# Optimization experiments

Measured on AMD Instinct MI355X. Metric: run time of the kernel, lower is better.

## Reference

```python
import jax, jax.numpy as jnp
import numpy as np

NEG_SLOPE_GAT = 0.2   # GATConv internal leaky_relu slope (PyG default)
NEG_SLOPE = 0.01      # nn.LeakyReLU default slope


def _gat(h_src_in, h_dst_in, src, dst, Wsrc, Wdst, a_s, a_d, b, n_dst, self_loops):
    """Single-head PyG-style GATConv: gather -> score -> edge softmax -> scatter-sum."""
    hs = h_src_in @ Wsrc            # [N_src, C]
    hd = h_dst_in @ Wdst            # [N_dst, C]
    if self_loops:                  # static flag; same node set on both sides
        loop = jnp.arange(n_dst, dtype=src.dtype)
        src = jnp.concatenate([src, loop])
        dst = jnp.concatenate([dst, loop])
    # attention logits per edge
    e = jax.nn.leaky_relu((hs @ a_s)[src] + (hd @ a_d)[dst], NEG_SLOPE_GAT)  # [E]
    # softmax over edges sharing a destination node
    m = jax.ops.segment_max(e, dst, num_segments=n_dst)
    ex = jnp.exp(e - m[dst])
    denom = jax.ops.segment_sum(ex, dst, num_segments=n_dst)
    alpha = ex / denom[dst]
    out = jax.ops.segment_sum(hs[src] * alpha[:, None], dst, num_segments=n_dst)
    return out + b


def setup_inputs() -> dict:
    key = jax.random.key(0)
    ks = iter(jax.random.split(key, 64))
    NB, NP = 100_000, 50_000
    E_bb, E_pp, E_bp = 800_000, 400_000, 400_000
    FB, FP, H, H2 = 32, 34, 64, 32
    rn = lambda shape, s=0.05: jax.random.normal(next(ks), shape, jnp.float32) * s
    d = {}
    d['x_b'] = rn((NB, FB), 1.0)
    d['x_p'] = rn((NP, FP), 1.0)
    d['ei_bb'] = jax.random.randint(next(ks), (2, E_bb), 0, NB, jnp.int32)
    d['ei_pp'] = jax.random.randint(next(ks), (2, E_pp), 0, NP, jnp.int32)
    d['ei_bp_src'] = jax.random.randint(next(ks), (E_bp,), 0, NB, jnp.int32)
    d['ei_bp_dst'] = jax.random.randint(next(ks), (E_bp,), 0, NP, jnp.int32)
    d['W_in_b'] = rn((FB, H)); d['b_in_b'] = jnp.zeros((H,), jnp.float32)
    d['W_in_p'] = rn((FP, H)); d['b_in_p'] = jnp.zeros((H,), jnp.float32)
    for tag, cin, cout in (('1', H, H), ('2', H, H2)):
        d['W_bb' + tag] = rn((cin, cout)); d['as_bb' + tag] = rn((cout,)); d['ad_bb' + tag] = rn((cout,)); d['b_bb' + tag] = jnp.zeros((cout,), jnp.float32)
        d['W_pp' + tag] = rn((cin, cout)); d['as_pp' + tag] = rn((cout,)); d['ad_pp' + tag] = rn((cout,)); d['b_pp' + tag] = jnp.zeros((cout,), jnp.float32)
        d['Ws_bp' + tag] = rn((cin, cout)); d['Wd_bp' + tag] = rn((cin, cout)); d['as_bp' + tag] = rn((cout,)); d['ad_bp' + tag] = rn((cout,)); d['b_bp' + tag] = jnp.zeros((cout,), jnp.float32)
    d['W_out'] = rn((H2, 1)); d['b_out'] = jnp.zeros((1,), jnp.float32)
    return d


def reference(x_b, x_p, ei_bb, ei_pp, ei_bp_src, ei_bp_dst,
              W_in_b, b_in_b, W_in_p, b_in_p,
              W_bb1, as_bb1, ad_bb1, b_bb1, W_pp1, as_pp1, ad_pp1, b_pp1,
              Ws_bp1, Wd_bp1, as_bp1, ad_bp1, b_bp1,
              W_bb2, as_bb2, ad_bb2, b_bb2, W_pp2, as_pp2, ad_pp2, b_pp2,
              Ws_bp2, Wd_bp2, as_bp2, ad_bp2, b_bp2,
              W_out, b_out):
    NB, NP = x_b.shape[0], x_p.shape[0]
    lr = lambda v: jax.nn.leaky_relu(v, NEG_SLOPE)
    # input projections (dropout is eval-mode identity)
    hb = lr(x_b @ W_in_b + b_in_b)
    hp = lr(x_p @ W_in_p + b_in_p)
    # hetero conv 1 (sum aggregation over relations sharing a dst type)
    ob = _gat(hb, hb, ei_bb[0], ei_bb[1], W_bb1, W_bb1, as_bb1, ad_bb1, b_bb1, NB, True)
    op = (_gat(hp, hp, ei_pp[0], ei_pp[1], W_pp1, W_pp1, as_pp1, ad_pp1, b_pp1, NP, True)
          + _gat(hb, hp, ei_bp_src, ei_bp_dst, Ws_bp1, Wd_bp1, as_bp1, ad_bp1, b_bp1, NP, False))
    hb, hp = lr(ob), lr(op)
    # hetero conv 2
    ob2 = _gat(hb, hb, ei_bb[0], ei_bb[1], W_bb2, W_bb2, as_bb2, ad_bb2, b_bb2, NB, True)
    op2 = (_gat(hp, hp, ei_pp[0], ei_pp[1], W_pp2, W_pp2, as_pp2, ad_pp2, b_pp2, NP, True)
           + _gat(hb, hp, ei_bp_src, ei_bp_dst, Ws_bp2, Wd_bp2, as_bp2, ad_bp2, b_bp2, NP, False))
    hp = lr(op2)
    return hp @ W_out + b_out  # [NP, 1]
```

## Files before the change

### kernel.cpp

```cpp
#include <hip/hip_runtime.h>
#include <hip/hip_bf16.h>
#include <cstdint>
#include <cstddef>


typedef __attribute__((ext_vector_type(8))) short short8;
typedef __attribute__((ext_vector_type(4))) float f32x4;
typedef unsigned int u32;
typedef __hip_bfloat16 bf16;

#define ABITS 9
#define CHUNKE 4096

static __device__ __forceinline__ float b2f(bf16 v) { return __bfloat162float(v); }

static __device__ __forceinline__ float ldf(const void* p, int i, int bf) {
    return bf ? __bfloat162float(((const bf16*)p)[i]) : ((const float*)p)[i];
}

static __device__ __forceinline__ short f2bs(float f) {
    bf16 h = __float2bfloat16(f);
    return *reinterpret_cast<short*>(&h);
}
static __device__ __forceinline__ float bs2f(short s) {
    bf16 h = *reinterpret_cast<bf16*>(&s);
    return __bfloat162float(h);
}
static __device__ __forceinline__ float lo16(u32 u) { return bs2f((short)(u & 0xffffu)); }
static __device__ __forceinline__ float hi16(u32 u) { return bs2f((short)(u >> 16)); }
static __device__ __forceinline__ u32 pack2(float x, float y) {
    return (u32)(unsigned short)f2bs(x) | ((u32)(unsigned short)f2bs(y) << 16);
}
static __device__ __forceinline__ float sel4(const float* a, int i) {
    return i == 0 ? a[0] : i == 1 ? a[1] : i == 2 ? a[2] : a[3];
}
static __device__ __forceinline__ float lrelu2(float x) { return x > 0.f ? x : 0.2f * x; }

__global__ __launch_bounds__(256) void k_bkt_hist(
    const int* __restrict__ bb_d, const int* __restrict__ pp_d,
    const int* __restrict__ bp_d, int* __restrict__ histM,
    const unsigned* __restrict__ probe_w, int* __restrict__ flag,
    int E_bb, int E_pp, int E_bp, int NB, int NP, int nbkt, int nblk)
{
    if (blockIdx.x == 0) {
        __shared__ int s_cnt;
        if (threadIdx.x == 0) s_cnt = 0;
        __syncthreads();
        int c = 0;
#pragma unroll
        for (int j = 0; j < 4; ++j) {
            unsigned u = probe_w[threadIdx.x * 4 + j];
            unsigned e = (u >> 7) & 0xffu;
            c += (e >= 100u && e <= 145u) ? 1 : 0;
        }
        atomicAdd(&s_cnt, c);
        __syncthreads();
        if (threadIdx.x == 0) *flag = (s_cnt > 614) ? 1 : 0;
    }
    __shared__ int h[1 << ABITS];
    for (int i = threadIdx.x; i < nbkt; i += 256) h[i] = 0;
    __syncthreads();
    int E_all = E_bb + E_pp + E_bp;
    int base = blockIdx.x * CHUNKE;
    int end = base + CHUNKE < E_all ? base + CHUNKE : E_all;
    for (int i = base + threadIdx.x; i < end; i += 256) {
        int d;
        if (i < E_bb) d = bb_d[i];
        else if (i < E_bb + E_pp) d = NB + pp_d[i - E_bb];
        else d = NB + NP + bp_d[i - E_bb - E_pp];
        atomicAdd(&h[d >> ABITS], 1);
    }
    __syncthreads();
    for (int i = threadIdx.x; i < nbkt; i += 256)
        histM[(size_t)i * nblk + blockIdx.x] = h[i];
}

__global__ __launch_bounds__(1024) void k_scan1(const int* __restrict__ deg,
                                                int* __restrict__ out,
                                                int* __restrict__ bsum, int n)
{
    __shared__ int wsum[16];
    int gid = blockIdx.x * 1024 + threadIdx.x;
    int lane = threadIdx.x & 63, wid = threadIdx.x >> 6;
    int v = (gid < n) ? deg[gid] : 0;
    int x = v;
#pragma unroll
    for (int off = 1; off < 64; off <<= 1) {
        int y = __shfl_up(x, off, 64);
        if (lane >= off) x += y;
    }
    if (lane == 63) wsum[wid] = x;
    __syncthreads();
    if (wid == 0 && lane < 16) {
        int w0 = wsum[lane];
#pragma unroll
        for (int off = 1; off < 16; off <<= 1) {
            int y = __shfl_up(w0, off, 16);
            if (lane >= off) w0 += y;
        }
        wsum[lane] = w0;
    }
    __syncthreads();
    int base = (wid > 0) ? wsum[wid - 1] : 0;
    int incl = base + x;
    if (gid < n) out[gid] = incl - v;
    if (threadIdx.x == 1023) bsum[blockIdx.x] = incl;
}

__global__ __launch_bounds__(1024) void k_scan2(int* __restrict__ bsum, int nb)
{
    __shared__ int wsum[16];
    int lane = threadIdx.x & 63, wid = threadIdx.x >> 6;
    int v = (threadIdx.x < nb) ? bsum[threadIdx.x] : 0;
    int x = v;
#pragma unroll
    for (int off = 1; off < 64; off <<= 1) {
        int y = __shfl_up(x, off, 64);
        if (lane >= off) x += y;
    }
    if (lane == 63) wsum[wid] = x;
    __syncthreads();
    if (wid == 0 && lane < 16) {
        int w0 = wsum[lane];
#pragma unroll
        for (int off = 1; off < 16; off <<= 1) {
            int y = __shfl_up(w0, off, 16);
            if (lane >= off) w0 += y;
        }
        wsum[lane] = w0;
    }
    __syncthreads();
    int base = (wid > 0) ? wsum[wid - 1] : 0;
    if (threadIdx.x < nb) bsum[threadIdx.x] = base + x - v;
}

__global__ __launch_bounds__(1024) void k_scan3(int* __restrict__ indptr,
                                                const int* __restrict__ bsum,
                                                int n, int E)
{
    int gid = blockIdx.x * 1024 + threadIdx.x;
    if (gid < n) indptr[gid] += bsum[blockIdx.x];
    if (gid == 0) indptr[n] = E;
}

__global__ __launch_bounds__(256) void k_bkt_scatter(
    const int* __restrict__ bb_s, const int* __restrict__ bb_d,
    const int* __restrict__ pp_s, const int* __restrict__ pp_d,
    const int* __restrict__ bp_s, const int* __restrict__ bp_d,
    const int* __restrict__ histS, unsigned* __restrict__ ebuf,
    int E_bb, int E_pp, int E_bp, int NB, int NP, int nbkt, int nblk)
{
    __shared__ int cur[1 << ABITS];
    for (int i = threadIdx.x; i < nbkt; i += 256)
        cur[i] = histS[(size_t)i * nblk + blockIdx.x];
    __syncthreads();
    int E_all = E_bb + E_pp + E_bp;
    int base = blockIdx.x * CHUNKE;
    int end = base + CHUNKE < E_all ? base + CHUNKE : E_all;
    for (int i = base + threadIdx.x; i < end; i += 256) {
        int s, d;
        if (i < E_bb) { s = bb_s[i]; d = bb_d[i]; }
        else if (i < E_bb + E_pp) { int j = i - E_bb; s = pp_s[j]; d = NB + pp_d[j]; }
        else { int j = i - E_bb - E_pp; s = bp_s[j]; d = NB + NP + bp_d[j]; }
        int p = atomicAdd(&cur[d >> ABITS], 1);
        ebuf[p] = ((unsigned)(d & ((1 << ABITS) - 1)) << 20) | (unsigned)s;
    }
}

__global__ __launch_bounds__(256) void k_finalize(
    const unsigned* __restrict__ ebuf, const int* __restrict__ histS,
    int* __restrict__ ip_all, int* __restrict__ sidx,
    int NALL, int E_all, int nbkt, int nblk)
{
    __shared__ int h[1 << ABITS];
    __shared__ int pre[1 << ABITS];
    __shared__ int wq[4];
    int b = blockIdx.x;
    int d0 = b << ABITS;
    int nloc = NALL - d0 < (1 << ABITS) ? NALL - d0 : (1 << ABITS);
    int t = threadIdx.x;
    for (int i = t; i < (1 << ABITS); i += 256) h[i] = 0;
    __syncthreads();
    int s0 = histS[(size_t)b * nblk];
    int s1 = histS[(size_t)(b + 1) * nblk];
    for (int i = s0 + t; i < s1; i += 256)
        atomicAdd(&h[ebuf[i] >> 20], 1);
    __syncthreads();
    int v0 = h[2 * t], v1 = h[2 * t + 1];
    int ps = v0 + v1;
    int lane = t & 63, wid = t >> 6;
    int x = ps;
#pragma unroll
    for (int off = 1; off < 64; off <<= 1) {
        int y = __shfl_up(x, off, 64);
        if (lane >= off) x += y;
    }
    if (lane == 63) wq[wid] = x;
    __syncthreads();
    if (t == 0) {
        int a = 0;
#pragma unroll
        for (int w = 0; w < 4; ++w) { int tmp = wq[w]; wq[w] = a; a += tmp; }
    }
    __syncthreads();
    int excl = wq[wid] + x - ps;
    pre[2 * t]     = excl;
    pre[2 * t + 1] = excl + v0;
    __syncthreads();
    for (int i = t; i < nloc; i += 256) ip_all[d0 + i] = s0 + pre[i];
    if (d0 + nloc == NALL && t == 0) ip_all[NALL] = E_all;
    for (int i = t; i < (1 << ABITS); i += 256) h[i] = s0 + pre[i];
    __syncthreads();
    for (int i = s0 + t; i < s1; i += 256) {
        unsigned e = ebuf[i];
        int p = atomicAdd(&h[e >> 20], 1);
        sidx[p] = (int)(e & 0xFFFFFu);
    }
}

template <int CIN>
static __device__ __forceinline__ void in_proj_body(
    short* WT, float* bl, int bid,
    const void* __restrict__ X, const void* __restrict__ W, const void* __restrict__ B,
    bf16* __restrict__ Y, int M, int bf)
{
    constexpr int KP = 40;
    for (int i = threadIdx.x; i < 64 * CIN; i += 256) {
        int n = i / CIN, k = i - n * CIN;
        WT[n * KP + k] = f2bs(ldf(W, k * 64 + n, bf));
    }
    if (threadIdx.x < 64) bl[threadIdx.x] = ldf(B, threadIdx.x, bf);
    __syncthreads();

    int lane = threadIdx.x & 63;
    int wv   = threadIdx.x >> 6;
    int m = lane & 15, quad = lane >> 4;
    int row0 = (bid * 4 + wv) * 16;
    if (row0 >= M) return;

    int arow = row0 + m; if (arow >= M) arow = M - 1;
    short8 a;
#pragma unroll
    for (int j = 0; j < 8; ++j)
        a[j] = f2bs(ldf(X, arow * CIN + quad * 8 + j, bf));

    f32x4 acc[4] = {};
#pragma unroll
    for (int tt = 0; tt < 4; ++tt) {
        short8 bfr = *(const short8*)&WT[((lane & 15) + 16 * tt) * KP + quad * 8];
        acc[tt] = __builtin_amdgcn_mfma_f32_16x16x32_bf16(a, bfr, acc[tt], 0, 0, 0);
// ... 4 lines not shown
#pragma unroll
        for (int r = 0; r < 4; ++r) {
            int row = row0 + quad * 4 + r; if (row >= M) row = M - 1;
            x32[r] = ldf(X, row * CIN + 32, bf);
            x33[r] = ldf(X, row * CIN + 33, bf);
        }
#pragma unroll
        for (int tt = 0; tt < 4; ++tt) {
            int col = (lane & 15) + 16 * tt;
            float w32 = bs2f(WT[col * KP + 32]);
            float w33 = bs2f(WT[col * KP + 33]);
#pragma unroll
            for (int r = 0; r < 4; ++r)
                acc[tt][r] += x32[r] * w32 + x33[r] * w33;
        }
    }

#pragma unroll
    for (int tt = 0; tt < 4; ++tt) {
        int col = (lane & 15) + 16 * tt;
        float bb = bl[col];
#pragma unroll
        for (int r = 0; r < 4; ++r) {
            int row = row0 + quad * 4 + r;
            if (row < M) {
                float v = acc[tt][r] + bb;
                v = v > 0.f ? v : 0.01f * v;
                Y[(size_t)row * 64 + col] = __float2bfloat16(v);
            }
        }
    }
}

__global__ __launch_bounds__(256) void k_in_proj_all(
    const void* __restrict__ Xb, const void* __restrict__ Wb, const void* __restrict__ Bb,
    bf16* __restrict__ Yb, int MB,
    const void* __restrict__ Xp, const void* __restrict__ Wp, const void* __restrict__ Bp,
    bf16* __restrict__ Yp, int MP, const int* __restrict__ flag)
{
    const int bf = *flag;
    __shared__ short WT[64 * 40];
    __shared__ float bl[64];
    int nbb = (MB + 63) >> 6;
    if (blockIdx.x < nbb) in_proj_body<32>(WT, bl, blockIdx.x, Xb, Wb, Bb, Yb, MB, bf);
    else                  in_proj_body<34>(WT, bl, blockIdx.x - nbb, Xp, Wp, Bp, Yp, MP, bf);
}

template <int N1, int N2, bool S1F, bool S2F>
static __device__ __forceinline__ void dual_body(
    short* WT, int bid, const bf16* __restrict__ H,
    const void* __restrict__ W1, const void* __restrict__ W2,
    const void* __restrict__ as1, const void* __restrict__ ad1,
    const void* __restrict__ as2, const void* __restrict__ ad2,
    bf16* __restrict__ HS1, bf16* __restrict__ HS2,
    float* __restrict__ SS1, float* __restrict__ SD1,
    float* __restrict__ SS2, float* __restrict__ SD2,
    int M, int bf)
{
    constexpr int KP = 72;
    constexpr int T1 = N1 / 16, T2 = N2 / 16, T = T1 + T2;
    for (int i = threadIdx.x; i < N1 * 64; i += 256) {
        int n = i >> 6, k = i & 63;
        WT[n * KP + k] = f2bs(ldf(W1, k * N1 + n, bf));
    }
    for (int i = threadIdx.x; i < N2 * 64; i += 256) {
        int n = i >> 6, k = i & 63;
        WT[(N1 + n) * KP + k] = f2bs(ldf(W2, k * N2 + n, bf));
    }
    __syncthreads();

    int lane = threadIdx.x & 63;
    int wv   = threadIdx.x >> 6;
    int m = lane & 15, quad = lane >> 4;
    int row0 = (bid * 4 + wv) * 16;
    if (row0 >= M) return;

    const short* Hs = (const short*)H;
    int arow = row0 + m; if (arow >= M) arow = M - 1;
// ... 126 lines not shown
            vs[r] += acc[tt][r] * asv[tt];
            vd[r] += acc[tt][r] * adv[tt];
        }
#pragma unroll
    for (int off = 1; off < 16; off <<= 1)
#pragma unroll
        for (int r = 0; r < 4; ++r) {
            vs[r] += __shfl_xor(vs[r], off);
            vd[r] += __shfl_xor(vd[r], off);
        }
    int c = lane & 15;
    if (c < 8) {
        int row = row0 + quad * 4 + (c & 3);
        if (row < M) {
            if (c < 4) SS[row] = sel4(vs, c & 3);
            else       SD[row] = sel4(vd, c & 3);
        }
    }

    if (STORE) {
#pragma unroll
        for (int tt = 0; tt < T; ++tt) {
            int col = (lane & 15) + 16 * tt;
#pragma unroll
            for (int r = 0; r < 4; ++r) {
                int row = row0 + quad * 4 + r;
                if (row < M)
                    HS[(size_t)row * N + col] = __float2bfloat16(acc[tt][r]);
            }
        }
    }
}

__global__ __launch_bounds__(256) void k_dual64_all(
    const bf16* __restrict__ hb,
    const void* W_bb1, const void* Ws_bp1,
    const void* as_bb1, const void* ad_bb1, const void* as_bp1, const void* ad_bp1,
    bf16* hs_bb, bf16* hs_bp,
    float* ss_bb, float* sd_bb, float* ss_bp, float* junkNB, int MB,
    const bf16* __restrict__ hp,
    const void* W_pp1, const void* Wd_bp1,
    const void* as_pp1, const void* ad_pp1,
    bf16* hs_pp, float* ss_pp, float* sd_pp, float* junkNP, float* sd_bp, int MP,
    const int* __restrict__ flag)
{
    const int bf = *flag;
    __shared__ short WT[128 * 72];
    int nbb = (MB + 63) >> 6;
    if (blockIdx.x < nbb)
        dual_body<64, 64, true, true>(WT, blockIdx.x, hb, W_bb1, Ws_bp1,
            as_bb1, ad_bb1, as_bp1, ad_bp1, hs_bb, hs_bp,
            ss_bb, sd_bb, ss_bp, junkNB, MB, bf);
    else
        dual_body<64, 64, true, false>(WT, blockIdx.x - nbb, hp, W_pp1, Wd_bp1,
            as_pp1, ad_pp1, as_bp1, ad_bp1, hs_pp, nullptr,
            ss_pp, sd_pp, junkNP, sd_bp, MP, bf);
}

__global__ __launch_bounds__(256) void k_proj2_all(
    const bf16* __restrict__ hp2,
    const void* W_pp2, const void* Wd_bp2,
    const void* as_pp2, const void* ad_pp2, const void* as_bp2, const void* ad_bp2,
    bf16* hs2_pp, float* ss2_pp, float* sd2_pp, float* junkNP, float* sd2_bp, int MP,
    const bf16* __restrict__ hb2,
    const void* Ws_bp2, bf16* hs2_bp, float* ss2_bp, float* junkNB, int MB,
    const int* __restrict__ flag)
{
    const int bf = *flag;
    __shared__ short WT[64 * 72];
    int npb = (MP + 63) >> 6;
    if (blockIdx.x < npb)
        dual_body<32, 32, true, false>(WT, blockIdx.x, hp2, W_pp2, Wd_bp2,
            as_pp2, ad_pp2, as_bp2, ad_bp2, hs2_pp, nullptr,
            ss2_pp, sd2_pp, junkNP, sd2_bp, MP, bf);
    else
        proj_body<32, true>(WT, blockIdx.x - npb, hb2, Ws_bp2,
            as_bp2, ad_bp2, hs2_bp, ss2_bp, junkNB, MB, bf);
}

static __device__ __forceinline__ void gather1_body(
    int bid, const int* __restrict__ ip, const int* __restrict__ si,
    const float* __restrict__ SS, const float* __restrict__ SD,
    const bf16* __restrict__ HS, const void* __restrict__ bias,
    bf16* __restrict__ OUT, int M, int bf)
{
    int lane = threadIdx.x & 63;
    int half = lane >> 5, hl = lane & 31;
    int d = bid * 4 + (threadIdx.x >> 6);
    if (d >= M) return;
    const u32* H32 = (const u32*)HS;
    float sdd = SD[d];
    float ax = 0.f, ay = 0.f, den = 0.f;
    if (half == 0) {
        float ex = __expf(lrelu2(SS[d] + sdd));
        u32 h = H32[(size_t)d * 32 + hl];
        ax = lo16(h) * ex; ay = hi16(h) * ex; den = ex;
    }
    int j1 = ip[d + 1];
    int j = ip[d] + half;
    for (; j + 2 < j1; j += 4) {
        int s0 = si[j], s1 = si[j + 2];
        u32 h0 = H32[(size_t)s0 * 32 + hl];
        u32 h1 = H32[(size_t)s1 * 32 + hl];
        float e0 = __expf(lrelu2(SS[s0] + sdd));
        float e1 = __expf(lrelu2(SS[s1] + sdd));
        ax += lo16(h0) * e0 + lo16(h1) * e1;
        ay += hi16(h0) * e0 + hi16(h1) * e1;
        den += e0 + e1;
    }
    if (j < j1) {
        int s0 = si[j];
        u32 h0 = H32[(size_t)s0 * 32 + hl];
        float e0 = __expf(lrelu2(SS[s0] + sdd));
        ax += lo16(h0) * e0; ay += hi16(h0) * e0; den += e0;
    }
    ax += __shfl_xor(ax, 32); ay += __shfl_xor(ay, 32); den += __shfl_xor(den, 32);
    if (half == 0) {
        float vx = ax / den + ldf(bias, 2 * hl, bf);
        float vy = ay / den + ldf(bias, 2 * hl + 1, bf);
        vx = vx > 0.f ? vx : 0.01f * vx;
        vy = vy > 0.f ? vy : 0.01f * vy;
        ((u32*)OUT)[(size_t)d * 32 + hl] = pack2(vx, vy);
    }
}

static __device__ __forceinline__ void gather2_body(
    int bid, const int* __restrict__ ip1, const int* __restrict__ si,
    const float* __restrict__ SS1, const float* __restrict__ SD1,
    const bf16* __restrict__ HS1,
    const int* __restrict__ ip2,
    const float* __restrict__ SS2, const float* __restrict__ SD2,
    const bf16* __restrict__ HS2,
    const void* __restrict__ b1, const void* __restrict__ b2,
    bf16* __restrict__ OUT, int M, int bf)
{
    int lane = threadIdx.x & 63;
    int half = lane >> 5, hl = lane & 31;
    int d = bid * 4 + (threadIdx.x >> 6);
    if (d >= M) return;
    const u32* H1 = (const u32*)HS1;
    const u32* H2 = (const u32*)HS2;
    float sdd = SD1[d];
    float a1x = 0.f, a1y = 0.f, den1 = 0.f;
    if (half == 0) {
        float ex = __expf(lrelu2(SS1[d] + sdd));
        u32 h = H1[(size_t)d * 32 + hl];
        a1x = lo16(h) * ex; a1y = hi16(h) * ex; den1 = ex;
    }
    int j1 = ip1[d + 1];
    int j = ip1[d] + half;
    for (; j + 2 < j1; j += 4) {
        int s0 = si[j], s1 = si[j + 2];
        u32 h0 = H1[(size_t)s0 * 32 + hl];
        u32 h1 = H1[(size_t)s1 * 32 + hl];
        float e0 = __expf(lrelu2(SS1[s0] + sdd));
        float e1 = __expf(lrelu2(SS1[s1] + sdd));
        a1x += lo16(h0) * e0 + lo16(h1) * e1;
        a1y += hi16(h0) * e0 + hi16(h1) * e1;
        den1 += e0 + e1;
    }
    if (j < j1) {
        int s0 = si[j];
        u32 h0 = H1[(size_t)s0 * 32 + hl];
        float e0 = __expf(lrelu2(SS1[s0] + sdd));
        a1x += lo16(h0) * e0; a1y += hi16(h0) * e0; den1 += e0;
    }
    float sdd2 = SD2[d];
    float a2x = 0.f, a2y = 0.f, den2 = 0.f;
    j1 = ip2[d + 1];
    j = ip2[d] + half;
    for (; j + 2 < j1; j += 4) {
        int s0 = si[j], s1 = si[j + 2];
        u32 h0 = H2[(size_t)s0 * 32 + hl];
        u32 h1 = H2[(size_t)s1 * 32 + hl];
        float e0 = __expf(lrelu2(SS2[s0] + sdd2));
        float e1 = __expf(lrelu2(SS2[s1] + sdd2));
        a2x += lo16(h0) * e0 + lo16(h1) * e1;
        a2y += hi16(h0) * e0 + hi16(h1) * e1;
        den2 += e0 + e1;
    }
    if (j < j1) {
        int s0 = si[j];
        u32 h0 = H2[(size_t)s0 * 32 + hl];
        float e0 = __expf(lrelu2(SS2[s0] + sdd2));
        a2x += lo16(h0) * e0; a2y += hi16(h0) * e0; den2 += e0;
    }
    a1x += __shfl_xor(a1x, 32); a1y += __shfl_xor(a1y, 32); den1 += __shfl_xor(den1, 32);
    a2x += __shfl_xor(a2x, 32); a2y += __shfl_xor(a2y, 32); den2 += __shfl_xor(den2, 32);
    if (half == 0) {
        float inv2 = den2 > 0.f ? 1.f / den2 : 0.f;
        float vx = a1x / den1 + a2x * inv2 + ldf(b1, 2 * hl, bf) + ldf(b2, 2 * hl, bf);
        float vy = a1y / den1 + a2y * inv2 + ldf(b1, 2 * hl + 1, bf) + ldf(b2, 2 * hl + 1, bf);
        vx = vx > 0.f ? vx : 0.01f * vx;
        vy = vy > 0.f ? vy : 0.01f * vy;
        ((u32*)OUT)[(size_t)d * 32 + hl] = pack2(vx, vy);
    }
}

__global__ __launch_bounds__(256) void k_gather12(
    const int* __restrict__ ip_bb, const int* __restrict__ si,
    const float* __restrict__ ss_bb, const float* __restrict__ sd_bb,
    const bf16* __restrict__ hs_bb, const void* __restrict__ b_bb1,
    bf16* __restrict__ hb2, int NB,
    const int* __restrict__ ip_pp, const int* __restrict__ ip_bp,
    const float* __restrict__ ss_pp, const float* __restrict__ sd_pp,
    const bf16* __restrict__ hs_pp,
    const float* __restrict__ ss_bp, const float* __restrict__ sd_bp,
    const bf16* __restrict__ hs_bp,
    const void* __restrict__ b_pp1, const void* __restrict__ b_bp1,
    bf16* __restrict__ hp2, int NP,
    const int* __restrict__ flag)
{
    const int bf = *flag;
    int nbb = (NB + 3) >> 2;
    if (blockIdx.x < nbb)
        gather1_body(blockIdx.x, ip_bb, si, ss_bb, sd_bb, hs_bb, b_bb1, hb2, NB, bf);
    else
        gather2_body(blockIdx.x - nbb, ip_pp, si, ss_pp, sd_pp, hs_pp,
                     ip_bp, ss_bp, sd_bp, hs_bp, b_pp1, b_bp1, hp2, NP, bf);
}

__global__ __launch_bounds__(256) void k_gather_out(
    const int* __restrict__ ip1, const int* __restrict__ si,
    const float* __restrict__ SS1, const float* __restrict__ SD1,
    const bf16* __restrict__ HS1,
    const int* __restrict__ ip2,
    const float* __restrict__ SS2, const float* __restrict__ SD2,
    const bf16* __restrict__ HS2,
    const void* __restrict__ b1, const void* __restrict__ b2,
    const void* __restrict__ Wout, const void* __restrict__ bout,
    void* __restrict__ OUT, int M, const int* __restrict__ flag)
{
    const int bf = *flag;
    int lane = threadIdx.x & 63;
    int q = lane >> 4, hl = lane & 15;
    int d = blockIdx.x * 4 + (threadIdx.x >> 6);
    if (d >= M) return;
    const u32* H1 = (const u32*)HS1;
    const u32* H2 = (const u32*)HS2;
    float sdd = SD1[d];
    float a1x = 0.f, a1y = 0.f, den1 = 0.f;
    if (q == 0) {
        float ex = __expf(lrelu2(SS1[d] + sdd));
        u32 h = H1[(size_t)d * 16 + hl];
        a1x = lo16(h) * ex; a1y = hi16(h) * ex; den1 = ex;
    }
    int j1 = ip1[d + 1];
    for (int j = ip1[d] + q; j < j1; j += 4) {
        int s0 = si[j];
        u32 h0 = H1[(size_t)s0 * 16 + hl];
        float e0 = __expf(lrelu2(SS1[s0] + sdd));
        a1x += lo16(h0) * e0; a1y += hi16(h0) * e0; den1 += e0;
// ... 41 lines not shown
    const void *W_bb1 = d_in[10], *as_bb1 = d_in[11], *ad_bb1 = d_in[12], *b_bb1 = d_in[13];
    const void *W_pp1 = d_in[14], *as_pp1 = d_in[15], *ad_pp1 = d_in[16], *b_pp1 = d_in[17];
    const void *Ws_bp1 = d_in[18], *Wd_bp1 = d_in[19], *as_bp1 = d_in[20], *ad_bp1 = d_in[21], *b_bp1 = d_in[22];
    const void *W_pp2 = d_in[27], *as_pp2 = d_in[28], *ad_pp2 = d_in[29], *b_pp2 = d_in[30];
    const void *Ws_bp2 = d_in[31], *Wd_bp2 = d_in[32], *as_bp2 = d_in[33], *ad_bp2 = d_in[34], *b_bp2 = d_in[35];
    const void *W_out = d_in[36], *b_out = d_in[37];

    const int NB   = in_sizes[0] / 32;
    const int NP   = in_sizes[1] / 34;
    const int E_bb = in_sizes[2] / 2;
    const int E_pp = in_sizes[3] / 2;
    const int E_bp = in_sizes[4];
    const int E_all = E_bb + E_pp + E_bp;
    const int NALL  = NB + 2 * NP;
    const int* bb_s = ei_bb;  const int* bb_d = ei_bb + E_bb;
    const int* pp_s = ei_pp;  const int* pp_d = ei_pp + E_pp;
    (void)ws_size; (void)n_in; (void)out_size;

    const int nbkt  = (NALL + (1 << ABITS) - 1) >> ABITS;
    const int nblk  = (E_all + CHUNKE - 1) / CHUNKE;
    const int nh    = nbkt * nblk;

    char* base = (char*)d_ws;
    size_t o = 0;
    auto alloc = [&](size_t bytes) { char* p = base + o; o += (bytes + 255) & ~(size_t)255; return p; };

    int* flag  = (int*)alloc(256);
    int* bsum  = (int*)alloc(1024 * 4);
    int* histM = (int*)alloc((size_t)nh * 4);
    int* histS = (int*)alloc((size_t)(nh + 1) * 4);
    int* ip_all = (int*)alloc((size_t)(NALL + 1) * 4);
    unsigned* ebuf = (unsigned*)alloc((size_t)E_all * 4);
    int* si_all = (int*)alloc((size_t)E_all * 4);
    float* ss_bb = (float*)alloc((size_t)NB * 4);
    float* sd_bb = (float*)alloc((size_t)NB * 4);
    float* ss_bp = (float*)alloc((size_t)NB * 4);
    float* ss_pp = (float*)alloc((size_t)NP * 4);
    float* sd_pp = (float*)alloc((size_t)NP * 4);
    float* sd_bp = (float*)alloc((size_t)NP * 4);
    float* ss2_bp = ss_bb;
    float* ss2_pp = ss_pp;
    float* sd2_pp = sd_pp;
    float* sd2_bp = sd_bp;
    float* junkNB = (float*)ebuf;
    float* junkNP = (float*)ebuf + NB;

    char* S1 = alloc((size_t)NB * 64 * 2);
    char* S2 = alloc((size_t)NP * 64 * 2);
    char* S3 = alloc((size_t)NB * 64 * 2);
    char* S4 = alloc((size_t)NB * 64 * 2);
    char* S5 = alloc((size_t)NB * 64 * 2);
    char* S6 = alloc((size_t)NP * 64 * 2);

    bf16* hb     = (bf16*)S1;
    bf16* hp     = (bf16*)S2;
    bf16* hs_bb  = (bf16*)S3;
    bf16* hb2    = (bf16*)S4;
    bf16* hs_bp  = (bf16*)S5;
    bf16* hs_pp  = (bf16*)S6;
    bf16* hp2    = (bf16*)S2;
    bf16* hs2_pp = (bf16*)S3;
    bf16* hs2_bp = (bf16*)S1;

    auto cdiv = [](int a, int b) { return (a + b - 1) / b; };

    k_bkt_hist<<<nblk, 256, 0, stream>>>(bb_d, pp_d, bp_d, histM,
                                         (const unsigned*)x_b, flag,
                                         E_bb, E_pp, E_bp, NB, NP, nbkt, nblk);
    int sb1 = cdiv(nh, 1024);
    k_scan1<<<sb1, 1024, 0, stream>>>(histM, histS, bsum, nh);
    k_scan2<<<1, 1024, 0, stream>>>(bsum, sb1);
    k_scan3<<<sb1, 1024, 0, stream>>>(histS, bsum, nh, E_all);
    k_bkt_scatter<<<nblk, 256, 0, stream>>>(bb_s, bb_d, pp_s, pp_d, bp_s, bp_d,
                                            histS, ebuf, E_bb, E_pp, E_bp, NB, NP, nbkt, nblk);
    k_finalize<<<nbkt, 256, 0, stream>>>(ebuf, histS, ip_all, si_all, NALL, E_all, nbkt, nblk);

    const int* ip_bb = ip_all;
    const int* ip_pp = ip_all + NB;
    const int* ip_bp = ip_all + NB + NP;

    k_in_proj_all<<<cdiv(NB, 64) + cdiv(NP, 64), 256, 0, stream>>>(
        x_b, W_in_b, b_in_b, hb, NB, x_p, W_in_p, b_in_p, hp, NP, flag);

    k_dual64_all<<<cdiv(NB, 64) + cdiv(NP, 64), 256, 0, stream>>>(
        hb, W_bb1, Ws_bp1, as_bb1, ad_bb1, as_bp1, ad_bp1,
        hs_bb, hs_bp, ss_bb, sd_bb, ss_bp, junkNB, NB,
        hp, W_pp1, Wd_bp1, as_pp1, ad_pp1,
        hs_pp, ss_pp, sd_pp, junkNP, sd_bp, NP, flag);

    k_gather12<<<cdiv(NB, 4) + cdiv(NP, 4), 256, 0, stream>>>(
        ip_bb, si_all, ss_bb, sd_bb, hs_bb, b_bb1, hb2, NB,
        ip_pp, ip_bp, ss_pp, sd_pp, hs_pp, ss_bp, sd_bp, hs_bp,
        b_pp1, b_bp1, hp2, NP, flag);

    k_proj2_all<<<cdiv(NP, 64) + cdiv(NB, 64), 256, 0, stream>>>(
        hp2, W_pp2, Wd_bp2, as_pp2, ad_pp2, as_bp2, ad_bp2,
        hs2_pp, ss2_pp, sd2_pp, junkNP, sd2_bp, NP,
        hb2, Ws_bp2, hs2_bp, ss2_bp, junkNB, NB, flag);

    k_gather_out<<<cdiv(NP, 4), 256, 0, stream>>>(
        ip_pp, si_all, ss2_pp, sd2_pp, hs2_pp,
        ip_bp, ss2_bp, sd2_bp, hs2_bp,
        b_pp2, b_bp2, W_out, b_out, d_out, NP, flag);
}
```

Before: 407.9 us.

## Fuse CSR build with projections and precompute layer-1 edge weights in finalize

```diff
diff --git a/kernel.cpp b/kernel.cpp
--- a/kernel.cpp
+++ b/kernel.cpp
@@ -10,7 +10,7 @@
 typedef __hip_bfloat16 bf16;
 
 #define ABITS 9
-#define CHUNKE 4096
+#define CHUNKE 8192
 
 static __device__ __forceinline__ float b2f(bf16 v) { return __bfloat162float(v); }
 
@@ -36,186 +36,21 @@
 }
 static __device__ __forceinline__ float lrelu2(float x) { return x > 0.f ? x : 0.2f * x; }
 
-__global__ __launch_bounds__(256) void k_bkt_hist(
-    const int* __restrict__ bb_d, const int* __restrict__ pp_d,
-    const int* __restrict__ bp_d, int* __restrict__ histM,
-    const unsigned* __restrict__ probe_w, int* __restrict__ flag,
-    int E_bb, int E_pp, int E_bp, int NB, int NP, int nbkt, int nblk)
-{
-    if (blockIdx.x == 0) {
-        __shared__ int s_cnt;
-        if (threadIdx.x == 0) s_cnt = 0;
-        __syncthreads();
-        int c = 0;
-#pragma unroll
-        for (int j = 0; j < 4; ++j) {
-            unsigned u = probe_w[threadIdx.x * 4 + j];
-            unsigned e = (u >> 7) & 0xffu;
-            c += (e >= 100u && e <= 145u) ? 1 : 0;
-        }
-        atomicAdd(&s_cnt, c);
-        __syncthreads();
-        if (threadIdx.x == 0) *flag = (s_cnt > 614) ? 1 : 0;
-    }
-    __shared__ int h[1 << ABITS];
-    for (int i = threadIdx.x; i < nbkt; i += 256) h[i] = 0;
-    __syncthreads();
-    int E_all = E_bb + E_pp + E_bp;
-    int base = blockIdx.x * CHUNKE;
-    int end = base + CHUNKE < E_all ? base + CHUNKE : E_all;
-    for (int i = base + threadIdx.x; i < end; i += 256) {
-        int d;
-        if (i < E_bb) d = bb_d[i];
-        else if (i < E_bb + E_pp) d = NB + pp_d[i - E_bb];
-        else d = NB + NP + bp_d[i - E_bb - E_pp];
-        atomicAdd(&h[d >> ABITS], 1);
-    }
-    __syncthreads();
-    for (int i = threadIdx.x; i < nbkt; i += 256)
-        histM[(size_t)i * nblk + blockIdx.x] = h[i];
-}
-
-__global__ __launch_bounds__(1024) void k_scan1(const int* __restrict__ deg,
-                                                int* __restrict__ out,
-                                                int* __restrict__ bsum, int n)
-{
-    __shared__ int wsum[16];
-    int gid = blockIdx.x * 1024 + threadIdx.x;
-    int lane = threadIdx.x & 63, wid = threadIdx.x >> 6;
-    int v = (gid < n) ? deg[gid] : 0;
-    int x = v;
-#pragma unroll
-    for (int off = 1; off < 64; off <<= 1) {
-        int y = __shfl_up(x, off, 64);
-        if (lane >= off) x += y;
-    }
-    if (lane == 63) wsum[wid] = x;
-    __syncthreads();
-    if (wid == 0 && lane < 16) {
-        int w0 = wsum[lane];
-#pragma unroll
-        for (int off = 1; off < 16; off <<= 1) {
-            int y = __shfl_up(w0, off, 16);
-            if (lane >= off) w0 += y;
-        }
-        wsum[lane] = w0;
-    }
-    __syncthreads();
-    int base = (wid > 0) ? wsum[wid - 1] : 0;
-    int incl = base + x;
-    if (gid < n) out[gid] = incl - v;
-    if (threadIdx.x == 1023) bsum[blockIdx.x] = incl;
-}
-
-__global__ __launch_bounds__(1024) void k_scan2(int* __restrict__ bsum, int nb)
-{
-    __shared__ int wsum[16];
-    int lane = threadIdx.x & 63, wid = threadIdx.x >> 6;
-    int v = (threadIdx.x < nb) ? bsum[threadIdx.x] : 0;
-    int x = v;
-#pragma unroll
-    for (int off = 1; off < 64; off <<= 1) {
-        int y = __shfl_up(x, off, 64);
-        if (lane >= off) x += y;
-    }
-    if (lane == 63) wsum[wid] = x;
-    __syncthreads();
-    if (wid == 0 && lane < 16) {
-        int w0 = wsum[lane];
-#pragma unroll
-        for (int off = 1; off < 16; off <<= 1) {
-            int y = __shfl_up(w0, off, 16);
-            if (lane >= off) w0 += y;
-        }
-        wsum[lane] = w0;
-    }
-    __syncthreads();
-    int base = (wid > 0) ? wsum[wid - 1] : 0;
-    if (threadIdx.x < nb) bsum[threadIdx.x] = base + x - v;
-}
-
-__global__ __launch_bounds__(1024) void k_scan3(int* __restrict__ indptr,
-                                                const int* __restrict__ bsum,
-                                                int n, int E)
-{
-    int gid = blockIdx.x * 1024 + threadIdx.x;
-    if (gid < n) indptr[gid] += bsum[blockIdx.x];
-    if (gid == 0) indptr[n] = E;
-}
-
-__global__ __launch_bounds__(256) void k_bkt_scatter(
-    const int* __restrict__ bb_s, const int* __restrict__ bb_d,
-    const int* __restrict__ pp_s, const int* __restrict__ pp_d,
-    const int* __restrict__ bp_s, const int* __restrict__ bp_d,
-    const int* __restrict__ histS, unsigned* __restrict__ ebuf,
-    int E_bb, int E_pp, int E_bp, int NB, int NP, int nbkt, int nblk)
-{
-    __shared__ int cur[1 << ABITS];
-    for (int i = threadIdx.x; i < nbkt; i += 256)
-        cur[i] = histS[(size_t)i * nblk + blockIdx.x];
-    __syncthreads();
-    int E_all = E_bb + E_pp + E_bp;
-    int base = blockIdx.x * CHUNKE;
-    int end = base + CHUNKE < E_all ? base + CHUNKE : E_all;
-    for (int i = base + threadIdx.x; i < end; i += 256) {
-        int s, d;
-        if (i < E_bb) { s = bb_s[i]; d = bb_d[i]; }
-        else if (i < E_bb + E_pp) { int j = i - E_bb; s = pp_s[j]; d = NB + pp_d[j]; }
-        else { int j = i - E_bb - E_pp; s = bp_s[j]; d = NB + NP + bp_d[j]; }
-        int p = atomicAdd(&cur[d >> ABITS], 1);
-        ebuf[p] = ((unsigned)(d & ((1 << ABITS) - 1)) << 20) | (unsigned)s;
-    }
-}
-
-__global__ __launch_bounds__(256) void k_finalize(
-    const unsigned* __restrict__ ebuf, const int* __restrict__ histS,
-    int* __restrict__ ip_all, int* __restrict__ sidx,
-    int NALL, int E_all, int nbkt, int nblk)
-{
-    __shared__ int h[1 << ABITS];
-    __shared__ int pre[1 << ABITS];
-    __shared__ int wq[4];
-    int b = blockIdx.x;
-    int d0 = b << ABITS;
-    int nloc = NALL - d0 < (1 << ABITS) ? NALL - d0 : (1 << ABITS);
-    int t = threadIdx.x;
-    for (int i = t; i < (1 << ABITS); i += 256) h[i] = 0;
-    __syncthreads();
-    int s0 = histS[(size_t)b * nblk];
-    int s1 = histS[(size_t)(b + 1) * nblk];
-    for (int i = s0 + t; i < s1; i += 256)
-        atomicAdd(&h[ebuf[i] >> 20], 1);
-    __syncthreads();
-    int v0 = h[2 * t], v1 = h[2 * t + 1];
-    int ps = v0 + v1;
-    int lane = t & 63, wid = t >> 6;
-    int x = ps;
-#pragma unroll
-    for (int off = 1; off < 64; off <<= 1) {
-        int y = __shfl_up(x, off, 64);
-        if (lane >= off) x += y;
-    }
-    if (lane == 63) wq[wid] = x;
-    __syncthreads();
-    if (t == 0) {
-        int a = 0;
-#pragma unroll
-        for (int w = 0; w < 4; ++w) { int tmp = wq[w]; wq[w] = a; a += tmp; }
-    }
-    __syncthreads();
-    int excl = wq[wid] + x - ps;
-    pre[2 * t]     = excl;
-    pre[2 * t + 1] = excl + v0;
-    __syncthreads();
-    for (int i = t; i < nloc; i += 256) ip_all[d0 + i] = s0 + pre[i];
-    if (d0 + nloc == NALL && t == 0) ip_all[NALL] = E_all;
-    for (int i = t; i < (1 << ABITS); i += 256) h[i] = s0 + pre[i];
-    __syncthreads();
-    for (int i = s0 + t; i < s1; i += 256) {
-        unsigned e = ebuf[i];
-        int p = atomicAdd(&h[e >> 20], 1);
-        sidx[p] = (int)(e & 0xFFFFFu);
-    }
+static __device__ __forceinline__ int probe_bf(const unsigned* __restrict__ w, int* cnt) {
+    if (threadIdx.x == 0) *cnt = 0;
+    __syncthreads();
+    int c = 0;
+#pragma unroll
+    for (int j = 0; j < 4; ++j) {
+        unsigned u = w[threadIdx.x * 4 + j];
+        unsigned e = (u >> 7) & 0xffu;
+        c += (e >= 100u && e <= 145u) ? 1 : 0;
+    }
+    atomicAdd(cnt, c);
+    __syncthreads();
+    int r = (*cnt > 614) ? 1 : 0;
+    __syncthreads();
+    return r;
 }
 
 template <int CIN>
@@ -286,18 +121,114 @@
     }
 }
 
-__global__ __launch_bounds__(256) void k_in_proj_all(
+__global__ __launch_bounds__(256) void k_hist_inproj(
+    const int* __restrict__ bb_d, const int* __restrict__ pp_d,
+    const int* __restrict__ bp_d, int* __restrict__ histM,
+    const unsigned* __restrict__ probe_w, int* __restrict__ flag,
+    int E_bb, int E_pp, int E_bp, int NB, int NP, int nbkt, int nblk,
     const void* __restrict__ Xb, const void* __restrict__ Wb, const void* __restrict__ Bb,
     bf16* __restrict__ Yb, int MB,
     const void* __restrict__ Xp, const void* __restrict__ Wp, const void* __restrict__ Bp,
-    bf16* __restrict__ Yp, int MP, const int* __restrict__ flag)
-{
-    const int bf = *flag;
+    bf16* __restrict__ Yp, int MP)
+{
     __shared__ short WT[64 * 40];
     __shared__ float bl[64];
-    int nbb = (MB + 63) >> 6;
-    if (blockIdx.x < nbb) in_proj_body<32>(WT, bl, blockIdx.x, Xb, Wb, Bb, Yb, MB, bf);
-    else                  in_proj_body<34>(WT, bl, blockIdx.x - nbb, Xp, Wp, Bp, Yp, MP, bf);
+    __shared__ int aux[1 << ABITS];
+    if ((int)blockIdx.x < nblk) {
+        if (blockIdx.x == 0) {
+            int b = probe_bf(probe_w, &aux[0]);
+            if (threadIdx.x == 0) *flag = b;
+        }
+        for (int i = threadIdx.x; i < nbkt; i += 256) aux[i] = 0;
+        __syncthreads();
+        int E_all = E_bb + E_pp + E_bp;
+        int base = blockIdx.x * CHUNKE;
+        int end = base + CHUNKE < E_all ? base + CHUNKE : E_all;
+        for (int i = base + threadIdx.x; i < end; i += 256) {
+            int d;
+            if (i < E_bb) d = bb_d[i];
+            else if (i < E_bb + E_pp) d = NB + pp_d[i - E_bb];
+            else d = NB + NP + bp_d[i - E_bb - E_pp];
+            atomicAdd(&aux[d >> ABITS], 1);
+        }
+        __syncthreads();
+        for (int i = threadIdx.x; i < nbkt; i += 256)
+            histM[(size_t)i * nblk + blockIdx.x] = aux[i];
+    } else {
+        int bfv = probe_bf(probe_w, &aux[0]);
+        int bid = blockIdx.x - nblk;
+        int nbb = (MB + 63) >> 6;
+        if (bid < nbb) in_proj_body<32>(WT, bl, bid, Xb, Wb, Bb, Yb, MB, bfv);
+        else           in_proj_body<34>(WT, bl, bid - nbb, Xp, Wp, Bp, Yp, MP, bfv);
+    }
+}
+
+__global__ __launch_bounds__(1024) void k_scan1(const int* __restrict__ deg,
+                                                int* __restrict__ out,
+                                                int* __restrict__ bsum, int n)
+{
+    __shared__ int wsum[16];
+    int gid = blockIdx.x * 1024 + threadIdx.x;
+    int lane = threadIdx.x & 63, wid = threadIdx.x >> 6;
+    int v = (gid < n) ? deg[gid] : 0;
+    int x = v;
+#pragma unroll
+    for (int off = 1; off < 64; off <<= 1) {
+        int y = __shfl_up(x, off, 64);
+        if (lane >= off) x += y;
+    }
+    if (lane == 63) wsum[wid] = x;
+    __syncthreads();
+    if (wid == 0 && lane < 16) {
+        int w0 = wsum[lane];
+#pragma unroll
+        for (int off = 1; off < 16; off <<= 1) {
+            int y = __shfl_up(w0, off, 16);
+            if (lane >= off) w0 += y;
+        }
+        wsum[lane] = w0;
+    }
+    __syncthreads();
+    int base = (wid > 0) ? wsum[wid - 1] : 0;
+    int incl = base + x;
+    if (gid < n) out[gid] = incl - v;
+    if (threadIdx.x == 1023) bsum[blockIdx.x] = incl;
+}
+
+__global__ __launch_bounds__(1024) void k_scan2(int* __restrict__ bsum, int nb)
+{
+    __shared__ int wsum[16];
+    int lane = threadIdx.x & 63, wid = threadIdx.x >> 6;
+    int v = (threadIdx.x < nb) ? bsum[threadIdx.x] : 0;
+    int x = v;
+#pragma unroll
+    for (int off = 1; off < 64; off <<= 1) {
+        int y = __shfl_up(x, off, 64);
+        if (lane >= off) x += y;
+    }
+    if (lane == 63) wsum[wid] = x;
+    __syncthreads();
+    if (wid == 0 && lane < 16) {
+        int w0 = wsum[lane];
+#pragma unroll
+        for (int off = 1; off < 16; off <<= 1) {
+            int y = __shfl_up(w0, off, 16);
+            if (lane >= off) w0 += y;
+        }
+        wsum[lane] = w0;
+    }
+    __syncthreads();
+    int base = (wid > 0) ? wsum[wid - 1] : 0;
+    if (threadIdx.x < nb) bsum[threadIdx.x] = base + x - v;
+}
+
+__global__ __launch_bounds__(1024) void k_scan3(int* __restrict__ indptr,
+                                                const int* __restrict__ bsum,
+                                                int n, int E)
+{
+    int gid = blockIdx.x * 1024 + threadIdx.x;
+    if (gid < n) indptr[gid] += bsum[blockIdx.x];
+    if (gid == 0) indptr[n] = E;
 }
 
 template <int N1, int N2, bool S1F, bool S2F>
@@ -490,7 +421,12 @@
     }
 }
 
-__global__ __launch_bounds__(256) void k_dual64_all(
+__global__ __launch_bounds__(256) void k_scatter_dual(
+    const int* __restrict__ bb_s, const int* __restrict__ bb_d,
+    const int* __restrict__ pp_s, const int* __restrict__ pp_d,
+    const int* __restrict__ bp_s, const int* __restrict__ bp_d,
+    const int* __restrict__ histS, unsigned* __restrict__ ebuf,
+    int E_bb, int E_pp, int E_bp, int NB, int NP, int nbkt, int nblk,
     const bf16* __restrict__ hb,
     const void* W_bb1, const void* Ws_bp1,
     const void* as_bb1, const void* ad_bb1, const void* as_bp1, const void* ad_bp1,
@@ -502,42 +438,103 @@
     bf16* hs_pp, float* ss_pp, float* sd_pp, float* junkNP, float* sd_bp, int MP,
     const int* __restrict__ flag)
 {
-    const int bf = *flag;
     __shared__ short WT[128 * 72];
-    int nbb = (MB + 63) >> 6;
-    if (blockIdx.x < nbb)
-        dual_body<64, 64, true, true>(WT, blockIdx.x, hb, W_bb1, Ws_bp1,
-            as_bb1, ad_bb1, as_bp1, ad_bp1, hs_bb, hs_bp,
-            ss_bb, sd_bb, ss_bp, junkNB, MB, bf);
-    else
-        dual_body<64, 64, true, false>(WT, blockIdx.x - nbb, hp, W_pp1, Wd_bp1,
-            as_pp1, ad_pp1, as_bp1, ad_bp1, hs_pp, nullptr,
-            ss_pp, sd_pp, junkNP, sd_bp, MP, bf);
-}
-
-__global__ __launch_bounds__(256) void k_proj2_all(
-    const bf16* __restrict__ hp2,
-    const void* W_pp2, const void* Wd_bp2,
-    const void* as_pp2, const void* ad_pp2, const void* as_bp2, const void* ad_bp2,
-    bf16* hs2_pp, float* ss2_pp, float* sd2_pp, float* junkNP, float* sd2_bp, int MP,
-    const bf16* __restrict__ hb2,
-    const void* Ws_bp2, bf16* hs2_bp, float* ss2_bp, float* junkNB, int MB,
-    const int* __restrict__ flag)
-{
-    const int bf = *flag;
-    __shared__ short WT[64 * 72];
-    int npb = (MP + 63) >> 6;
-    if (blockIdx.x < npb)
-        dual_body<32, 32, true, false>(WT, blockIdx.x, hp2, W_pp2, Wd_bp2,
-            as_pp2, ad_pp2, as_bp2, ad_bp2, hs2_pp, nullptr,
-            ss2_pp, sd2_pp, junkNP, sd2_bp, MP, bf);
-    else
-        proj_body<32, true>(WT, blockIdx.x - npb, hb2, Ws_bp2,
-            as_bp2, ad_bp2, hs2_bp, ss2_bp, junkNB, MB, bf);
+    if ((int)blockIdx.x < nblk) {
+        int* cur = (int*)WT;
+        for (int i = threadIdx.x; i < nbkt; i += 256)
+            cur[i] = histS[(size_t)i * nblk + blockIdx.x];
+        __syncthreads();
+        int E_all = E_bb + E_pp + E_bp;
+        int base = blockIdx.x * CHUNKE;
+        int end = base + CHUNKE < E_all ? base + CHUNKE : E_all;
+        for (int i = base + threadIdx.x; i < end; i += 256) {
+            int s, d;
+            if (i < E_bb) { s = bb_s[i]; d = bb_d[i]; }
+            else if (i < E_bb + E_pp) { int j = i - E_bb; s = pp_s[j]; d = NB + pp_d[j]; }
+            else { int j = i - E_bb - E_pp; s = bp_s[j]; d = NB + NP + bp_d[j]; }
+            int p = atomicAdd(&cur[d >> ABITS], 1);
+            ebuf[p] = ((unsigned)(d & ((1 << ABITS) - 1)) << 20) | (unsigned)s;
+        }
+    } else {
+        const int bfv = *flag;
+        int bid = blockIdx.x - nblk;
+        int nbb = (MB + 63) >> 6;
+        if (bid < nbb)
+            dual_body<64, 64, true, true>(WT, bid, hb, W_bb1, Ws_bp1,
+                as_bb1, ad_bb1, as_bp1, ad_bp1, hs_bb, hs_bp,
+                ss_bb, sd_bb, ss_bp, junkNB, MB, bfv);
+        else
+            dual_body<64, 64, true, false>(WT, bid - nbb, hp, W_pp1, Wd_bp1,
+                as_pp1, ad_pp1, as_bp1, ad_bp1, hs_pp, nullptr,
+                ss_pp, sd_pp, junkNP, sd_bp, MP, bfv);
+    }
+}
+
+__global__ __launch_bounds__(256) void k_finalize(
+    const unsigned* __restrict__ ebuf, const int* __restrict__ histS,
+    int* __restrict__ ip_all, int* __restrict__ sidx, float* __restrict__ wedge,
+    const float* __restrict__ ss_bb, const float* __restrict__ sd_bb,
+    const float* __restrict__ ss_pp, const float* __restrict__ sd_pp,
+    const float* __restrict__ ss_bp, const float* __restrict__ sd_bp,
+    int NB, int NP, int NALL, int E_all, int nbkt, int nblk)
+{
+    __shared__ int h[1 << ABITS];
+    __shared__ int pre[1 << ABITS];
+    __shared__ int wq[4];
+    int b = blockIdx.x;
+    int d0 = b << ABITS;
+    int nloc = NALL - d0 < (1 << ABITS) ? NALL - d0 : (1 << ABITS);
+    int t = threadIdx.x;
+    for (int i = t; i < (1 << ABITS); i += 256) h[i] = 0;
+    __syncthreads();
+    int s0 = histS[(size_t)b * nblk];
+    int s1 = histS[(size_t)(b + 1) * nblk];
+    for (int i = s0 + t; i < s1; i += 256)
+        atomicAdd(&h[ebuf[i] >> 20], 1);
+    __syncthreads();
+    int v0 = h[2 * t], v1 = h[2 * t + 1];
+    int ps = v0 + v1;
+    int lane = t & 63, wid = t >> 6;
+    int x = ps;
+#pragma unroll
+    for (int off = 1; off < 64; off <<= 1) {
+        int y = __shfl_up(x, off, 64);
+        if (lane >= off) x += y;
+    }
+    if (lane == 63) wq[wid] = x;
+    __syncthreads();
+    if (t == 0) {
+        int a = 0;
+#pragma unroll
+        for (int w = 0; w < 4; ++w) { int tmp = wq[w]; wq[w] = a; a += tmp; }
+    }
+    __syncthreads();
+    int excl = wq[wid] + x - ps;
+    pre[2 * t]     = excl;
+    pre[2 * t + 1] = excl + v0;
+    __syncthreads();
+    for (int i = t; i < nloc; i += 256) ip_all[d0 + i] = s0 + pre[i];
+    if (d0 + nloc == NALL && t == 0) ip_all[NALL] = E_all;
+    for (int i = t; i < (1 << ABITS); i += 256) h[i] = s0 + pre[i];
+    __syncthreads();
+    for (int i = s0 + t; i < s1; i += 256) {
+        unsigned e = ebuf[i];
+        int dl = (int)(e >> 20);
+        int src = (int)(e & 0xFFFFFu);
+        int p = atomicAdd(&h[dl], 1);
+        int d = d0 + dl;
+        float ssv, sdv;
+        if (d < NB)           { ssv = ss_bb[src]; sdv = sd_bb[d]; }
+        else if (d < NB + NP) { ssv = ss_pp[src]; sdv = sd_pp[d - NB]; }
+        else                  { ssv = ss_bp[src]; sdv = sd_bp[d - NB - NP]; }
+        sidx[p] = src;
+        wedge[p] = __expf(lrelu2(ssv + sdv));
+    }
 }
 
 static __device__ __forceinline__ void gather1_body(
     int bid, const int* __restrict__ ip, const int* __restrict__ si,
+    const float* __restrict__ w,
     const float* __restrict__ SS, const float* __restrict__ SD,
     const bf16* __restrict__ HS, const void* __restrict__ bias,
     bf16* __restrict__ OUT, int M, int bf)
@@ -547,10 +544,9 @@
     int d = bid * 4 + (threadIdx.x >> 6);
     if (d >= M) return;
     const u32* H32 = (const u32*)HS;
-    float sdd = SD[d];
     float ax = 0.f, ay = 0.f, den = 0.f;
     if (half == 0) {
-        float ex = __expf(lrelu2(SS[d] + sdd));
+        float ex = __expf(lrelu2(SS[d] + SD[d]));
         u32 h = H32[(size_t)d * 32 + hl];
         ax = lo16(h) * ex; ay = hi16(h) * ex; den = ex;
     }
@@ -558,18 +554,17 @@
     int j = ip[d] + half;
     for (; j + 2 < j1; j += 4) {
         int s0 = si[j], s1 = si[j + 2];
+        float e0 = w[j], e1 = w[j + 2];
         u32 h0 = H32[(size_t)s0 * 32 + hl];
         u32 h1 = H32[(size_t)s1 * 32 + hl];
-        float e0 = __expf(lrelu2(SS[s0] + sdd));
-        float e1 = __expf(lrelu2(SS[s1] + sdd));
         ax += lo16(h0) * e0 + lo16(h1) * e1;
         ay += hi16(h0) * e0 + hi16(h1) * e1;
         den += e0 + e1;
     }
     if (j < j1) {
         int s0 = si[j];
+        float e0 = w[j];
         u32 h0 = H32[(size_t)s0 * 32 + hl];
-        float e0 = __expf(lrelu2(SS[s0] + sdd));
         ax += lo16(h0) * e0; ay += hi16(h0) * e0; den += e0;
     }
     ax += __shfl_xor(ax, 32); ay += __shfl_xor(ay, 32); den += __shfl_xor(den, 32);
@@ -584,11 +579,10 @@
 
 static __device__ __forceinline__ void gather2_body(
     int bid, const int* __restrict__ ip1, const int* __restrict__ si,
+    const float* __restrict__ w,
     const float* __restrict__ SS1, const float* __restrict__ SD1,
     const bf16* __restrict__ HS1,
-    const int* __restrict__ ip2,
-    const float* __restrict__ SS2, const float* __restrict__ SD2,
-    const bf16* __restrict__ HS2,
+    const int* __restrict__ ip2, const bf16* __restrict__ HS2,
     const void* __restrict__ b1, const void* __restrict__ b2,
     bf16* __restrict__ OUT, int M, int bf)
 {
@@ -598,10 +592,9 @@
     if (d >= M) return;
     const u32* H1 = (const u32*)HS1;
     const u32* H2 = (const u32*)HS2;
-    float sdd = SD1[d];
     float a1x = 0.f, a1y = 0.f, den1 = 0.f;
     if (half == 0) {
-        float ex = __expf(lrelu2(SS1[d] + sdd));
+        float ex = __expf(lrelu2(SS1[d] + SD1[d]));
         u32 h = H1[(size_t)d * 32 + hl];
         a1x = lo16(h) * ex; a1y = hi16(h) * ex; den1 = ex;
     }
@@ -609,38 +602,35 @@
     int j = ip1[d] + half;
     for (; j + 2 < j1; j += 4) {
         int s0 = si[j], s1 = si[j + 2];
+        float e0 = w[j], e1 = w[j + 2];
         u32 h0 = H1[(size_t)s0 * 32 + hl];
         u32 h1 = H1[(size_t)s1 * 32 + hl];
-        float e0 = __expf(lrelu2(SS1[s0] + sdd));
-        float e1 = __expf(lrelu2(SS1[s1] + sdd));
         a1x += lo16(h0) * e0 + lo16(h1) * e1;
         a1y += hi16(h0) * e0 + hi16(h1) * e1;
         den1 += e0 + e1;
     }
     if (j < j1) {
         int s0 = si[j];
+        float e0 = w[j];
         u32 h0 = H1[(size_t)s0 * 32 + hl];
-        float e0 = __expf(lrelu2(SS1[s0] + sdd));
         a1x += lo16(h0) * e0; a1y += hi16(h0) * e0; den1 += e0;
     }
-    float sdd2 = SD2[d];
     float a2x = 0.f, a2y = 0.f, den2 = 0.f;
     j1 = ip2[d + 1];
     j = ip2[d] + half;
     for (; j + 2 < j1; j += 4) {
         int s0 = si[j], s1 = si[j + 2];
+        float e0 = w[j], e1 = w[j + 2];
         u32 h0 = H2[(size_t)s0 * 32 + hl];
         u32 h1 = H2[(size_t)s1 * 32 + hl];
-        float e0 = __expf(lrelu2(SS2[s0] + sdd2));
-        float e1 = __expf(lrelu2(SS2[s1] + sdd2));
         a2x += lo16(h0) * e0 + lo16(h1) * e1;
         a2y += hi16(h0) * e0 + hi16(h1) * e1;
         den2 += e0 + e1;
     }
     if (j < j1) {
         int s0 = si[j];
+        float e0 = w[j];
         u32 h0 = H2[(size_t)s0 * 32 + hl];
-        float e0 = __expf(lrelu2(SS2[s0] + sdd2));
         a2x += lo16(h0) * e0; a2y += hi16(h0) * e0; den2 += e0;
     }
     a1x += __shfl_xor(a1x, 32); a1y += __shfl_xor(a1y, 32); den1 += __shfl_xor(den1, 32);
@@ -657,25 +647,45 @@
 
 __global__ __launch_bounds__(256) void k_gather12(
     const int* __restrict__ ip_bb, const int* __restrict__ si,
+    const float* __restrict__ wedge,
     const float* __restrict__ ss_bb, const float* __restrict__ sd_bb,
     const bf16* __restrict__ hs_bb, const void* __restrict__ b_bb1,
     bf16* __restrict__ hb2, int NB,
     const int* __restrict__ ip_pp, const int* __restrict__ ip_bp,
     const float* __restrict__ ss_pp, const float* __restrict__ sd_pp,
-    const bf16* __restrict__ hs_pp,
-    const float* __restrict__ ss_bp, const float* __restrict__ sd_bp,
-    const bf16* __restrict__ hs_bp,
+    const bf16* __restrict__ hs_pp, const bf16* __restrict__ hs_bp,
     const void* __restrict__ b_pp1, const void* __restrict__ b_bp1,
     bf16* __restrict__ hp2, int NP,
     const int* __restrict__ flag)
 {
     const int bf = *flag;
     int nbb = (NB + 3) >> 2;
-    if (blockIdx.x < nbb)
-        gather1_body(blockIdx.x, ip_bb, si, ss_bb, sd_bb, hs_bb, b_bb1, hb2, NB, bf);
+    if ((int)blockIdx.x < nbb)
+        gather1_body(blockIdx.x, ip_bb, si, wedge, ss_bb, sd_bb, hs_bb, b_bb1, hb2, NB, bf);
     else
-        gather2_body(blockIdx.x - nbb, ip_pp, si, ss_pp, sd_pp, hs_pp,
-                     ip_bp, ss_bp, sd_bp, hs_bp, b_pp1, b_bp1, hp2, NP, bf);
+        gather2_body(blockIdx.x - nbb, ip_pp, si, wedge, ss_pp, sd_pp, hs_pp,
+                     ip_bp, hs_bp, b_pp1, b_bp1, hp2, NP, bf);
+}
+
+__global__ __launch_bounds__(256) void k_proj2_all(
+    const bf16* __restrict__ hp2,
+    const void* W_pp2, const void* Wd_bp2,
+    const void* as_pp2, const void* ad_pp2, const void* as_bp2, const void* ad_bp2,
+    bf16* hs2_pp, float* ss2_pp, float* sd2_pp, float* junkNP, float* sd2_bp, int MP,
+    const bf16* __restrict__ hb2,
+    const void* Ws_bp2, bf16* hs2_bp, float* ss2_bp, float* junkNB, int MB,
+    const int* __restrict__ flag)
+{
+    const int bf = *flag;
+    __shared__ short WT[64 * 72];
+    int npb = (MP + 63) >> 6;
+    if ((int)blockIdx.x < npb)
+        dual_body<32, 32, true, false>(WT, blockIdx.x, hp2, W_pp2, Wd_bp2,
+            as_pp2, ad_pp2, as_bp2, ad_bp2, hs2_pp, nullptr,
+            ss2_pp, sd2_pp, junkNP, sd2_bp, MP, bf);
+    else
+        proj_body<32, true>(WT, blockIdx.x - npb, hb2, Ws_bp2,
+            as_bp2, ad_bp2, hs2_bp, ss2_bp, junkNB, MB, bf);
 }
 
 __global__ __launch_bounds__(256) void k_gather_out(
@@ -783,18 +793,19 @@
     int* ip_all = (int*)alloc((size_t)(NALL + 1) * 4);
     unsigned* ebuf = (unsigned*)alloc((size_t)E_all * 4);
     int* si_all = (int*)alloc((size_t)E_all * 4);
+    float* wedge = (float*)alloc((size_t)E_all * 4);
     float* ss_bb = (float*)alloc((size_t)NB * 4);
     float* sd_bb = (float*)alloc((size_t)NB * 4);
     float* ss_bp = (float*)alloc((size_t)NB * 4);
     float* ss_pp = (float*)alloc((size_t)NP * 4);
     float* sd_pp = (float*)alloc((size_t)NP * 4);
     float* sd_bp = (float*)alloc((size_t)NP * 4);
+    float* junkNB = (float*)alloc((size_t)NB * 4);
+    float* junkNP = (float*)alloc((size_t)NP * 4);
     float* ss2_bp = ss_bb;
     float* ss2_pp = ss_pp;
     float* sd2_pp = sd_pp;
     float* sd2_bp = sd_bp;
-    float* junkNB = (float*)ebuf;
-    float* junkNP = (float*)ebuf + NB;
 
     char* S1 = alloc((size_t)NB * 64 * 2);
     char* S2 = alloc((size_t)NP * 64 * 2);
@@ -815,33 +826,35 @@
 
     auto cdiv = [](int a, int b) { return (a + b - 1) / b; };
 
-    k_bkt_hist<<<nblk, 256, 0, stream>>>(bb_d, pp_d, bp_d, histM,
-                                         (const unsigned*)x_b, flag,
-                                         E_bb, E_pp, E_bp, NB, NP, nbkt, nblk);
+    const int* ip_bb = ip_all;
+    const int* ip_pp = ip_all + NB;
+    const int* ip_bp = ip_all + NB + NP;
+
+    k_hist_inproj<<<nblk + cdiv(NB, 64) + cdiv(NP, 64), 256, 0, stream>>>(
+        bb_d, pp_d, bp_d, histM, (const unsigned*)x_b, flag,
+        E_bb, E_pp, E_bp, NB, NP, nbkt, nblk,
+        x_b, W_in_b, b_in_b, hb, NB, x_p, W_in_p, b_in_p, hp, NP);
+
     int sb1 = cdiv(nh, 1024);
     k_scan1<<<sb1, 1024, 0, stream>>>(histM, histS, bsum, nh);
     k_scan2<<<1, 1024, 0, stream>>>(bsum, sb1);
     k_scan3<<<sb1, 1024, 0, stream>>>(histS, bsum, nh, E_all);
-    k_bkt_scatter<<<nblk, 256, 0, stream>>>(bb_s, bb_d, pp_s, pp_d, bp_s, bp_d,
-                                            histS, ebuf, E_bb, E_pp, E_bp, NB, NP, nbkt, nblk);
-    k_finalize<<<nbkt, 256, 0, stream>>>(ebuf, histS, ip_all, si_all, NALL, E_all, nbkt, nblk);
-
-    const int* ip_bb = ip_all;
-    const int* ip_pp = ip_all + NB;
-    const int* ip_bp = ip_all + NB + NP;
-
-    k_in_proj_all<<<cdiv(NB, 64) + cdiv(NP, 64), 256, 0, stream>>>(
-        x_b, W_in_b, b_in_b, hb, NB, x_p, W_in_p, b_in_p, hp, NP, flag);
-
-    k_dual64_all<<<cdiv(NB, 64) + cdiv(NP, 64), 256, 0, stream>>>(
+
+    k_scatter_dual<<<nblk + cdiv(NB, 64) + cdiv(NP, 64), 256, 0, stream>>>(
+        bb_s, bb_d, pp_s, pp_d, bp_s, bp_d, histS, ebuf,
+        E_bb, E_pp, E_bp, NB, NP, nbkt, nblk,
         hb, W_bb1, Ws_bp1, as_bb1, ad_bb1, as_bp1, ad_bp1,
         hs_bb, hs_bp, ss_bb, sd_bb, ss_bp, junkNB, NB,
         hp, W_pp1, Wd_bp1, as_pp1, ad_pp1,
         hs_pp, ss_pp, sd_pp, junkNP, sd_bp, NP, flag);
 
+    k_finalize<<<nbkt, 256, 0, stream>>>(ebuf, histS, ip_all, si_all, wedge,
+                                         ss_bb, sd_bb, ss_pp, sd_pp, ss_bp, sd_bp,
+                                         NB, NP, NALL, E_all, nbkt, nblk);
+
     k_gather12<<<cdiv(NB, 4) + cdiv(NP, 4), 256, 0, stream>>>(
-        ip_bb, si_all, ss_bb, sd_bb, hs_bb, b_bb1, hb2, NB,
-        ip_pp, ip_bp, ss_pp, sd_pp, hs_pp, ss_bp, sd_bp, hs_bp,
+        ip_bb, si_all, wedge, ss_bb, sd_bb, hs_bb, b_bb1, hb2, NB,
+        ip_pp, ip_bp, ss_pp, sd_pp, hs_pp, hs_bp,
         b_pp1, b_bp1, hp2, NP, flag);
 
     k_proj2_all<<<cdiv(NP, 64) + cdiv(NB, 64), 256, 0, stream>>>(
```

Measured after the change: 396.7 us. -2.8%, faster.
